# Optimization experiments

Hardware: AMD Instinct MI355X
Metric: run time of the kernel (lower is better)

## Reference

```python
import jax, jax.numpy as jnp
import numpy as np

B, NB, BS, F = 4, 16, 256, 1024   # batch, num_blocks, block_size, features
H, D = 16, 64                     # heads, head_dim
ROPE = 32                         # rope_rotary_dims


def rotate_every_two(x):
    x1 = x[..., ::2]
    x2 = x[..., 1::2]
    return jnp.stack([-x2, x1], axis=-1).reshape(x.shape)


def apply_rope(x, num_blocks, block_size):
    # x: [B, NB, BS, H, rope_dim]
    rope_dim = x.shape[-1]
    inv_freq = 1.0 / 10000.0 ** (jnp.arange(0, rope_dim, 2, dtype=jnp.float32) / rope_dim)
    pos = jnp.arange(num_blocks * block_size, dtype=jnp.float32)
    ang = pos[:, None] * inv_freq[None, :]                       # [S, rope_dim/2]
    sin = jnp.sin(ang).reshape(num_blocks, block_size, rope_dim // 2)
    cos = jnp.cos(ang).reshape(num_blocks, block_size, rope_dim // 2)
    sin = jnp.repeat(sin[None, :, :, None, :], 2, axis=-1)       # [1, NB, BS, 1, rope_dim]
    cos = jnp.repeat(cos[None, :, :, None, :], 2, axis=-1)
    return x * cos + rotate_every_two(x) * sin


def setup_inputs() -> dict:
    key = jax.random.key(0)
    ks = jax.random.split(key, 8)
    s_in = 1.0 / np.sqrt(F)
    s_out = 1.0 / np.sqrt(H * D)
    return {
        "inputs_q": jax.random.normal(ks[0], (B, NB, BS, F), jnp.float32),
        "inputs_kv": jax.random.normal(ks[1], (B, NB, BS, F), jnp.float32),
        "Wq": jax.random.normal(ks[2], (F, H, D), jnp.float32) * s_in,
        "bq": jnp.zeros((H, D), jnp.float32),
        "Wk": jax.random.normal(ks[3], (F, H, D), jnp.float32) * s_in,
        "bk": jnp.zeros((H, D), jnp.float32),
        "Wv": jax.random.normal(ks[4], (F, H, D), jnp.float32) * s_in,
        "bv": jnp.zeros((H, D), jnp.float32),
        "Wo": jax.random.normal(ks[5], (H, D, F), jnp.float32) * s_out,
        "bo": jnp.zeros((F,), jnp.float32),
    }


def reference(inputs_q, inputs_kv, Wq, bq, Wk, bk, Wv, bv, Wo, bo):
    # QKV projections: [B, NB, BS, F] x [F, H, D] -> [B, NB, BS, H, D]
    q = jnp.einsum("bnsf,fhd->bnshd", inputs_q, Wq) + bq
    k = jnp.einsum("bnsf,fhd->bnshd", inputs_kv, Wk) + bk
    v = jnp.einsum("bnsf,fhd->bnshd", inputs_kv, Wv) + bv

    # RoPE on first ROPE dims of head_dim (intended semantics per docstring)
    q_rot, q_pass = q[..., :ROPE], q[..., ROPE:]
    k_rot, k_pass = k[..., :ROPE], k[..., ROPE:]
    q = jnp.concatenate([apply_rope(q_rot, NB, BS), q_pass], axis=-1)
    k = jnp.concatenate([apply_rope(k_rot, NB, BS), k_pass], axis=-1)

    # block-local dot-product attention (flax nn.dot_product_attention semantics)
    q = q / jnp.sqrt(jnp.asarray(D, q.dtype))
    scores = jnp.einsum("bnqhd,bnkhd->bnhqk", q, k)              # [B, NB, H, BS, BS]
    weights = jax.nn.softmax(scores, axis=-1)
    x = jnp.einsum("bnhqk,bnkhd->bnqhd", weights, v)             # [B, NB, BS, H, D]

    # output projection over (heads, head_dim)
    out = jnp.einsum("bnqhd,hdf->bnqf", x, Wo) + bo              # [B, NB, BS, F]
    return out
```

## Files before the change

### kernel.cpp

```cpp
#include <hip/hip_runtime.h>

typedef __attribute__((ext_vector_type(4))) float f32x4;
typedef __attribute__((ext_vector_type(8))) short s16x8;
typedef __attribute__((ext_vector_type(4))) unsigned short u16x4;

struct F2 { float c, s; };

__device__ __forceinline__ unsigned short f2b(float f) {
  unsigned u = __builtin_bit_cast(unsigned, f);
  u += 0x7FFFu + ((u >> 16) & 1u);
  return (unsigned short)(u >> 16);
}
__device__ __forceinline__ void gll16(const void* g, void* l) {
  __builtin_amdgcn_global_load_lds(
      (const __attribute__((address_space(1))) unsigned int*)g,
      (__attribute__((address_space(3))) unsigned int*)l, 16, 0, 0);
}
__device__ __forceinline__ f32x4 mfma16(s16x8 a, s16x8 b, f32x4 c) {
  return __builtin_amdgcn_mfma_f32_16x16x32_bf16(a, b, c, 0, 0, 0);
}

__global__ void k_prep(const float* __restrict__ Xq, const float* __restrict__ Xkv,
                       unsigned short* __restrict__ Xqb, unsigned short* __restrict__ Xkvb,
                       F2* __restrict__ tab) {
  int b = blockIdx.x;
  if (b < 4096) {
    const float* src = (b < 2048) ? Xq : Xkv;
    unsigned short* dst = (b < 2048) ? Xqb : Xkvb;
    int i = (b & 2047) * 256 + threadIdx.x;
    for (; i < 4194304; i += 2048 * 256) {
      f32x4 v = ((const f32x4*)src)[i];
      u16x4 o;
      o.x = f2b(v.x); o.y = f2b(v.y); o.z = f2b(v.z); o.w = f2b(v.w);
      ((u16x4*)dst)[i] = o;
    }
  } else {
    int idx = (b - 4096) * 256 + threadIdx.x;
    int pos = idx >> 4, fi = idx & 15;
    double inv = exp((double)fi * (-9.210340371976184 / 16.0));
    double a = (double)pos * inv;
    F2 r; r.c = (float)cos(a); r.s = (float)sin(a);
    tab[idx] = r;
  }
}

__global__ void k_transpose(const float* __restrict__ wq,
                            const float* __restrict__ wk,
                            const float* __restrict__ wv,
                            const float* __restrict__ wo,
                            unsigned short* __restrict__ wtqkv,
                            unsigned short* __restrict__ wto) {
  __shared__ unsigned short tile[32][33];
  int z = blockIdx.z;
  const float* src = (z == 0) ? wq : (z == 1) ? wk : (z == 2) ? wv : wo;
  unsigned short* dst = (z < 3) ? (wtqkv + (size_t)z * 1048576) : wto;
  int bx = blockIdx.x * 32, by = blockIdx.y * 32;
  tile[threadIdx.y][threadIdx.x] = f2b(src[(size_t)(by + threadIdx.y) * 1024 + bx + threadIdx.x]);
  __syncthreads();
  dst[(size_t)(bx + threadIdx.y) * 1024 + by + threadIdx.x] = tile[threadIdx.x][threadIdx.y];
}

__device__ __forceinline__ void gemm_core(
    const unsigned short* __restrict__ Ag, const unsigned short* __restrict__ Bg,
    int m0, int n0, unsigned short* Sh, f32x4 (&acc)[8][4]) {
  const int tid = threadIdx.x, wid = tid >> 6, lane = tid & 63;
  const int fr = lane & 15, fg = lane >> 4, f7 = fr & 7;
  const int wm = wid >> 2, wn = wid & 3;
  const int rowoff = lane >> 3;
  const int lanecol = ((lane & 7) ^ rowoff) * 8;
  const int g0 = (fg ^ f7) * 8, g1 = ((4 + fg) ^ f7) * 8;

  auto SA = [&](int T, int ah) {
    unsigned short* dstb = Sh + (T & 1) * 32768;
#pragma unroll
    for (int i = 0; i < 2; ++i) {
      int rloc = ah * 128 + (wid * 2 + i) * 8;
      gll16(Ag + (size_t)(m0 + rloc + rowoff) * 1024 + T * 64 + lanecol, dstb + rloc * 64);
    }
  };
  auto SB = [&](int T, int bh) {
    unsigned short* dstb = Sh + (T & 1) * 32768 + 16384;
#pragma unroll
    for (int i = 0; i < 2; ++i) {
      int rloc = bh * 128 + (wid * 2 + i) * 8;
      gll16(Bg + (size_t)(n0 + rloc + rowoff) * 1024 + T * 64 + lanecol, dstb + rloc * 64);
    }
  };

  SA(0, 0); SA(0, 1); SB(0, 0); SB(0, 1); SA(1, 0); SA(1, 1);
  asm volatile("s_waitcnt vmcnt(4)" ::: "memory");
  __builtin_amdgcn_sched_barrier(0);
  __builtin_amdgcn_s_barrier();

  for (int t = 0; t < 16; ++t) {
    const unsigned short* bufA = Sh + (t & 1) * 32768;
    const unsigned short* bufB = bufA + 16384;
    s16x8 a0[4][2], a1[4][2], b0[2][2], b1[2][2];
#pragma unroll
    for (int mf = 0; mf < 4; ++mf) {
      const unsigned short* r = &bufA[(wm * 128 + mf * 16 + fr) * 64];
      a0[mf][0] = *(const s16x8*)&r[g0];
      a0[mf][1] = *(const s16x8*)&r[g1];
    }
#pragma unroll
    for (int nf = 0; nf < 2; ++nf) {
      const unsigned short* r = &bufB[(wn * 64 + nf * 16 + fr) * 64];
      b0[nf][0] = *(const s16x8*)&r[g0];
      b0[nf][1] = *(const s16x8*)&r[g1];
    }
    if (t + 1 < 16) SB(t + 1, 0);
    __builtin_amdgcn_s_barrier();
    asm volatile("s_waitcnt lgkmcnt(0)" ::: "memory");
    __builtin_amdgcn_sched_barrier(0);
    __builtin_amdgcn_s_setprio(1);
#pragma unroll
    for (int mf = 0; mf < 4; ++mf)
#pragma unroll
      for (int nf = 0; nf < 2; ++nf) {
        acc[mf][nf] = mfma16(a0[mf][0], b0[nf][0], acc[mf][nf]);
        acc[mf][nf] = mfma16(a0[mf][1], b0[nf][1], acc[mf][nf]);
      }
    __builtin_amdgcn_s_setprio(0);
    __builtin_amdgcn_s_barrier();
#pragma unroll
    for (int mf = 0; mf < 4; ++mf) {
      const unsigned short* r = &bufA[(wm * 128 + 64 + mf * 16 + fr) * 64];
      a1[mf][0] = *(const s16x8*)&r[g0];
      a1[mf][1] = *(const s16x8*)&r[g1];
    }
    if (t + 1 < 16) SB(t + 1, 1);
    __builtin_amdgcn_s_barrier();
    asm volatile("s_waitcnt lgkmcnt(0)" ::: "memory");
    __builtin_amdgcn_sched_barrier(0);
    __builtin_amdgcn_s_setprio(1);
#pragma unroll
    for (int mf = 0; mf < 4; ++mf)
#pragma unroll
      for (int nf = 0; nf < 2; ++nf) {
        acc[4 + mf][nf] = mfma16(a1[mf][0], b0[nf][0], acc[4 + mf][nf]);
        acc[4 + mf][nf] = mfma16(a1[mf][1], b0[nf][1], acc[4 + mf][nf]);
      }
    __builtin_amdgcn_s_setprio(0);
    __builtin_amdgcn_s_barrier();
#pragma unroll
    for (int nf = 0; nf < 2; ++nf) {
      const unsigned short* r = &bufB[(wn * 64 + 32 + nf * 16 + fr) * 64];
      b1[nf][0] = *(const s16x8*)&r[g0];
      b1[nf][1] = *(const s16x8*)&r[g1];
    }
    if (t + 2 < 16) SA(t + 2, 0);
    __builtin_amdgcn_s_barrier();
    asm volatile("s_waitcnt lgkmcnt(0)" ::: "memory");
    __builtin_amdgcn_sched_barrier(0);
    __builtin_amdgcn_s_setprio(1);
#pragma unroll
    for (int mf = 0; mf < 4; ++mf)
#pragma unroll
      for (int nf = 0; nf < 2; ++nf) {
        acc[4 + mf][2 + nf] = mfma16(a1[mf][0], b1[nf][0], acc[4 + mf][2 + nf]);
        acc[4 + mf][2 + nf] = mfma16(a1[mf][1], b1[nf][1], acc[4 + mf][2 + nf]);
      }
    __builtin_amdgcn_s_setprio(0);
    __builtin_amdgcn_s_barrier();
    if (t + 2 < 16) SA(t + 2, 1);
    if (t < 14) asm volatile("s_waitcnt vmcnt(4)" ::: "memory");
    else        asm volatile("s_waitcnt vmcnt(0)" ::: "memory");
    __builtin_amdgcn_sched_barrier(0);
    __builtin_amdgcn_s_barrier();
    __builtin_amdgcn_s_setprio(1);
#pragma unroll
    for (int mf = 0; mf < 4; ++mf)
#pragma unroll
      for (int nf = 0; nf < 2; ++nf) {
        acc[mf][2 + nf] = mfma16(a0[mf][0], b1[nf][0], acc[mf][2 + nf]);
        acc[mf][2 + nf] = mfma16(a0[mf][1], b1[nf][1], acc[mf][2 + nf]);
      }
    __builtin_amdgcn_s_setprio(0);
    __builtin_amdgcn_s_barrier();
  }
}

__global__ __launch_bounds__(512, 1) void k_qkv(
    const unsigned short* __restrict__ Xq,
    const unsigned short* __restrict__ Xkv,
    const unsigned short* __restrict__ WT,
    const float* __restrict__ bq,
    const float* __restrict__ bk,
    const float* __restrict__ bv,
    const F2* __restrict__ tab,
    unsigned short* __restrict__ qbuf,
    unsigned short* __restrict__ kbuf,
    unsigned short* __restrict__ vbuf) {
  __shared__ __align__(16) unsigned short S[65536];
  int bid = blockIdx.x;
  int swz = (bid & 7) * 96 + (bid >> 3);
  int mt = swz / 12, nt = swz % 12;
  int m0 = mt * 256, n0 = nt * 256;
  int which = n0 >> 10;
  const unsigned short* X = (which == 0) ? Xq : Xkv;
  const float* bias = (which == 0) ? bq : (which == 1) ? bk : bv;
  unsigned short* dst = (which == 0) ? qbuf : (which == 1) ? kbuf : vbuf;
  int n0l = n0 & 1023;
  int tid = threadIdx.x, wid = tid >> 6, lane = tid & 63;
  int fr = lane & 15, fg = lane >> 4;
  int wm = wid >> 2, wn = wid & 3;

  f32x4 acc[8][4] = {};
  gemm_core(X, WT, m0, n0, S, acc);

  unsigned short* W = S + wid * 8192;
  int hh = (n0l + wn * 64) >> 6;
  int bn = m0 >> 8;
#pragma unroll
  for (int nf = 0; nf < 4; ++nf) {
    int d = nf * 16 + fr;
    int col = n0l + wn * 64 + d;
    float bz = bias[col];
    bool rope = (which < 2) && (nf < 2);
#pragma unroll
    for (int mf = 0; mf < 8; ++mf) {
#pragma unroll
      for (int j = 0; j < 4; ++j) {
        int row = mf * 16 + fg * 4 + j;
        int mg = m0 + wm * 128 + row;
        float v = acc[mf][nf][j] + bz;
        if (rope) {
          float p = __shfl_xor(v, 1);
          F2 cs = tab[(mg & 4095) * 16 + (d >> 1)];
          v = (d & 1) ? fmaf(v, cs.c, p * cs.s) : fmaf(v, cs.c, -(p * cs.s));
        }
        if (which == 0) v *= 0.125f;
        W[row * 64 + (((d >> 3) ^ (row & 7)) << 3) + (d & 7)] = f2b(v);
      }
    }
  }
  asm volatile("s_waitcnt lgkmcnt(0)" ::: "memory");
  __builtin_amdgcn_sched_barrier(0);
  size_t gbase = ((size_t)(bn * 16 + hh) * 256 + wm * 128) * 64;
#pragma unroll
  for (int it = 0; it < 16; ++it) {
    int r = it * 8 + (lane >> 3);
    int ch = (lane & 7) ^ (r & 7);
    s16x8 vv = *(const s16x8*)&W[r * 64 + ch * 8];
    *(s16x8*)&dst[gbase + r * 64 + (lane & 7) * 8] = vv;
  }
}

__global__ __launch_bounds__(512, 1) void k_attn(
    const unsigned short* __restrict__ qbuf,
    const unsigned short* __restrict__ kbuf,
    const unsigned short* __restrict__ vbuf,
    unsigned short* __restrict__ xbuf) {
  __shared__ __align__(16) unsigned short Kl[256 * 64];
  __shared__ __align__(16) unsigned short Vt[64 * 264];
  __shared__ __align__(16) unsigned short Pl[8][16 * 264];
  int gb = blockIdx.x;
  size_t base = (size_t)gb * (256 * 64);
  const unsigned short* Q = qbuf + base;
  const unsigned short* K = kbuf + base;
  const unsigned short* V = vbuf + base;
  int bn = gb >> 4, h = gb & 15;
  int tid = threadIdx.x, wid = tid >> 6, lane = tid & 63;
  int fr = lane & 15, fg = lane >> 4;

#pragma unroll
  for (int tt = 0; tt < 4; ++tt) {
    int t = wid * 4 + tt;
    int r = t * 8 + (lane >> 3);
    int csrc = (lane & 7) ^ (r & 7);
    gll16(K + r * 64 + csrc * 8, &Kl[t * 512]);
  }
  {
    int rv = tid >> 1, chalf = (tid & 1) * 32;
#pragma unroll
    for (int c8 = 0; c8 < 4; ++c8) {
      s16x8 vv = *(const s16x8*)&V[rv * 64 + chalf + c8 * 8];
#pragma unroll
      for (int j = 0; j < 8; ++j)
        Vt[(chalf + c8 * 8 + j) * 264 + rv] = (unsigned short)vv[j];
    }
  }
  __syncthreads();

  unsigned short* P = Pl[wid];
  int f7 = fr & 7;
  int c0 = (fg ^ f7) * 8;
  int c1 = ((4 + fg) ^ f7) * 8;
  for (int mtile = 0; mtile < 2; ++mtile) {
    int q0 = wid * 32 + mtile * 16;
    s16x8 qa0 = *(const s16x8*)&Q[(q0 + fr) * 64 + fg * 8];
    s16x8 qa1 = *(const s16x8*)&Q[(q0 + fr) * 64 + 32 + fg * 8];
    f32x4 sc[16] = {};
#pragma unroll
    for (int nt = 0; nt < 16; ++nt) {
      int rr = nt * 16 + fr;
      s16x8 kb0 = *(const s16x8*)&Kl[rr * 64 + c0];
      sc[nt] = mfma16(qa0, kb0, sc[nt]);
      s16x8 kb1 = *(const s16x8*)&Kl[rr * 64 + c1];
      sc[nt] = mfma16(qa1, kb1, sc[nt]);
    }
    float rs[4];
#pragma unroll
    for (int j = 0; j < 4; ++j) {
      float m = sc[0][j];
#pragma unroll
      for (int nt = 1; nt < 16; ++nt) m = fmaxf(m, sc[nt][j]);
      m = fmaxf(m, __shfl_xor(m, 1));
      m = fmaxf(m, __shfl_xor(m, 2));
      m = fmaxf(m, __shfl_xor(m, 4));
      m = fmaxf(m, __shfl_xor(m, 8));
      float sum = 0.f;
#pragma unroll
      for (int nt = 0; nt < 16; ++nt) {
        float p = __expf(sc[nt][j] - m);
        sum += p;
        P[(fg * 4 + j) * 264 + nt * 16 + fr] = f2b(p);
      }
      sum += __shfl_xor(sum, 1);
      sum += __shfl_xor(sum, 2);
      sum += __shfl_xor(sum, 4);
      sum += __shfl_xor(sum, 8);
      rs[j] = 1.0f / sum;
    }
    f32x4 o[4] = {};
#pragma unroll
    for (int ks = 0; ks < 8; ++ks) {
      s16x8 pa = *(const s16x8*)&P[fr * 264 + ks * 32 + fg * 8];
#pragma unroll
      for (int nt = 0; nt < 4; ++nt) {
        s16x8 vb = *(const s16x8*)&Vt[(nt * 16 + fr) * 264 + ks * 32 + fg * 8];
        o[nt] = mfma16(pa, vb, o[nt]);
      }
    }
#pragma unroll
    for (int nt = 0; nt < 4; ++nt)
#pragma unroll
      for (int j = 0; j < 4; ++j) {
        int srow = q0 + fg * 4 + j;
        int d = nt * 16 + fr;
        xbuf[((size_t)(bn * 256 + srow)) * 1024 + h * 64 + d] = f2b(o[nt][j] * rs[j]);
      }
  }
}

__global__ __launch_bounds__(512, 1) void k_out(
    const unsigned short* __restrict__ Xb,
    const unsigned short* __restrict__ WT,
    const float* __restrict__ bo,
    float* __restrict__ out) {
  __shared__ __align__(16) unsigned short S[65536];
  int bid = blockIdx.x;
  int swz = (bid & 7) * 32 + (bid >> 3);
  int mt = swz >> 2, nt = swz & 3;
  int m0 = mt * 256, n0 = nt * 256;
  int tid = threadIdx.x, wid = tid >> 6, lane = tid & 63;
  int fr = lane & 15, fg = lane >> 4;
  int wm = wid >> 2, wn = wid & 3;

  f32x4 acc[8][4] = {};
  gemm_core(Xb, WT, m0, n0, S, acc);

  float* Wf = (float*)S + wid * 4096;
#pragma unroll
  for (int p = 0; p < 2; ++p) {
#pragma unroll
    for (int nf = 0; nf < 4; ++nf) {
      int d = nf * 16 + fr;
      float bz = bo[n0 + wn * 64 + d];
#pragma unroll
      for (int mf = 0; mf < 4; ++mf) {
#pragma unroll
        for (int j = 0; j < 4; ++j) {
          int row = mf * 16 + fg * 4 + j;
          Wf[row * 64 + d] = acc[p * 4 + mf][nf][j] + bz;
        }
      }
    }
    asm volatile("s_waitcnt lgkmcnt(0)" ::: "memory");
    __builtin_amdgcn_sched_barrier(0);
#pragma unroll
    for (int it = 0; it < 16; ++it) {
      int r = it * 4 + (lane >> 4);
      f32x4 vv = *(const f32x4*)&Wf[r * 64 + (lane & 15) * 4];
      int mg = m0 + wm * 128 + p * 64 + r;
      *(f32x4*)&out[(size_t)mg * 1024 + n0 + wn * 64 + (lane & 15) * 4] = vv;
    }
    asm volatile("s_waitcnt lgkmcnt(0)" ::: "memory");
    __builtin_amdgcn_sched_barrier(0);
  }
}

extern "C" void kernel_launch(void* const* d_in, const int* in_sizes, int n_in,
                              void* d_out, int out_size, void* d_ws, size_t ws_size,
                              hipStream_t stream) {
  const float* Xq  = (const float*)d_in[0];
  const float* Xkv = (const float*)d_in[1];
  const float* Wq  = (const float*)d_in[2];
  const float* bq  = (const float*)d_in[3];
  const float* Wk  = (const float*)d_in[4];
  const float* bk  = (const float*)d_in[5];
  const float* Wv  = (const float*)d_in[6];
  const float* bv  = (const float*)d_in[7];
  const float* Wo  = (const float*)d_in[8];
  const float* bo  = (const float*)d_in[9];
  float* out = (float*)d_out;

  char* ws = (char*)d_ws;
  size_t off = 0;
  F2* tab = (F2*)(ws + off);                           off += (size_t)65536 * sizeof(F2);
  unsigned short* WTqkv = (unsigned short*)(ws + off); off += (size_t)3 * 1048576 * 2;
  unsigned short* WTo   = (unsigned short*)(ws + off); off += (size_t)1048576 * 2;
  unsigned short* Xqb   = (unsigned short*)(ws + off); off += (size_t)16777216 * 2;
  unsigned short* Xkvb  = (unsigned short*)(ws + off); off += (size_t)16777216 * 2;
  unsigned short* qb = (unsigned short*)(ws + off); off += (size_t)16777216 * 2;
  unsigned short* kb = (unsigned short*)(ws + off); off += (size_t)16777216 * 2;
  unsigned short* vb = (unsigned short*)(ws + off); off += (size_t)16777216 * 2;
  unsigned short* xb = Xqb;

  k_prep<<<4352, 256, 0, stream>>>(Xq, Xkv, Xqb, Xkvb, tab);
  k_transpose<<<dim3(32, 32, 4), dim3(32, 32), 0, stream>>>(Wq, Wk, Wv, Wo, WTqkv, WTo);
  k_qkv<<<768, 512, 0, stream>>>(Xqb, Xkvb, WTqkv, bq, bk, bv, tab, qb, kb, vb);
  k_attn<<<1024, 512, 0, stream>>>(qb, kb, vb, xb);
  k_out<<<256, 512, 0, stream>>>(xb, WTo, bo, out);
}
```

Before: 279.2 us.

## Use 16 waves per GEMM block with smaller per-wave tiles

Result: no change. 282.5 us (+1.2%).

```diff
diff --git a/kernel.cpp b/kernel.cpp
--- a/kernel.cpp
+++ b/kernel.cpp
@@ -62,43 +62,39 @@
 
 __device__ __forceinline__ void gemm_core(
     const unsigned short* __restrict__ Ag, const unsigned short* __restrict__ Bg,
-    int m0, int n0, unsigned short* Sh, f32x4 (&acc)[8][4]) {
+    int m0, int n0, unsigned short* Sh, f32x4 (&acc)[4][4]) {
   const int tid = threadIdx.x, wid = tid >> 6, lane = tid & 63;
   const int fr = lane & 15, fg = lane >> 4, f7 = fr & 7;
   const int wm = wid >> 2, wn = wid & 3;
-  const int rowoff = lane >> 3;
-  const int lanecol = ((lane & 7) ^ rowoff) * 8;
   const int g0 = (fg ^ f7) * 8, g1 = ((4 + fg) ^ f7) * 8;
+  const int scp = lane & 7;
+  const int srow = wid * 8 + (lane >> 3);
 
   auto SA = [&](int T, int ah) {
     unsigned short* dstb = Sh + (T & 1) * 32768;
-#pragma unroll
-    for (int i = 0; i < 2; ++i) {
-      int rloc = ah * 128 + (wid * 2 + i) * 8;
-      gll16(Ag + (size_t)(m0 + rloc + rowoff) * 1024 + T * 64 + lanecol, dstb + rloc * 64);
-    }
+    int row = ah * 128 + srow;
+    gll16(Ag + (size_t)(m0 + row) * 1024 + T * 64 + (scp ^ (row & 7)) * 8,
+          dstb + (ah * 128 + wid * 8) * 64);
   };
   auto SB = [&](int T, int bh) {
     unsigned short* dstb = Sh + (T & 1) * 32768 + 16384;
-#pragma unroll
-    for (int i = 0; i < 2; ++i) {
-      int rloc = bh * 128 + (wid * 2 + i) * 8;
-      gll16(Bg + (size_t)(n0 + rloc + rowoff) * 1024 + T * 64 + lanecol, dstb + rloc * 64);
-    }
+    int row = bh * 128 + srow;
+    gll16(Bg + (size_t)(n0 + row) * 1024 + T * 64 + (scp ^ (row & 7)) * 8,
+          dstb + (bh * 128 + wid * 8) * 64);
   };
 
   SA(0, 0); SA(0, 1); SB(0, 0); SB(0, 1); SA(1, 0); SA(1, 1);
-  asm volatile("s_waitcnt vmcnt(4)" ::: "memory");
+  asm volatile("s_waitcnt vmcnt(2)" ::: "memory");
   __builtin_amdgcn_sched_barrier(0);
   __builtin_amdgcn_s_barrier();
 
   for (int t = 0; t < 16; ++t) {
     const unsigned short* bufA = Sh + (t & 1) * 32768;
     const unsigned short* bufB = bufA + 16384;
-    s16x8 a0[4][2], a1[4][2], b0[2][2], b1[2][2];
-#pragma unroll
-    for (int mf = 0; mf < 4; ++mf) {
-      const unsigned short* r = &bufA[(wm * 128 + mf * 16 + fr) * 64];
+    s16x8 a0[2][2], a1[2][2], b0[2][2], b1[2][2];
+#pragma unroll
+    for (int mf = 0; mf < 2; ++mf) {
+      const unsigned short* r = &bufA[(wm * 64 + mf * 16 + fr) * 64];
       a0[mf][0] = *(const s16x8*)&r[g0];
       a0[mf][1] = *(const s16x8*)&r[g1];
     }
@@ -114,7 +110,7 @@
     __builtin_amdgcn_sched_barrier(0);
     __builtin_amdgcn_s_setprio(1);
 #pragma unroll
-    for (int mf = 0; mf < 4; ++mf)
+    for (int mf = 0; mf < 2; ++mf)
 #pragma unroll
       for (int nf = 0; nf < 2; ++nf) {
         acc[mf][nf] = mfma16(a0[mf][0], b0[nf][0], acc[mf][nf]);
@@ -123,8 +119,8 @@
     __builtin_amdgcn_s_setprio(0);
     __builtin_amdgcn_s_barrier();
 #pragma unroll
-    for (int mf = 0; mf < 4; ++mf) {
-      const unsigned short* r = &bufA[(wm * 128 + 64 + mf * 16 + fr) * 64];
+    for (int mf = 0; mf < 2; ++mf) {
+      const unsigned short* r = &bufA[(wm * 64 + 32 + mf * 16 + fr) * 64];
       a1[mf][0] = *(const s16x8*)&r[g0];
       a1[mf][1] = *(const s16x8*)&r[g1];
     }
@@ -134,11 +130,11 @@
     __builtin_amdgcn_sched_barrier(0);
     __builtin_amdgcn_s_setprio(1);
 #pragma unroll
-    for (int mf = 0; mf < 4; ++mf)
+    for (int mf = 0; mf < 2; ++mf)
 #pragma unroll
       for (int nf = 0; nf < 2; ++nf) {
-        acc[4 + mf][nf] = mfma16(a1[mf][0], b0[nf][0], acc[4 + mf][nf]);
-        acc[4 + mf][nf] = mfma16(a1[mf][1], b0[nf][1], acc[4 + mf][nf]);
+        acc[2 + mf][nf] = mfma16(a1[mf][0], b0[nf][0], acc[2 + mf][nf]);
+        acc[2 + mf][nf] = mfma16(a1[mf][1], b0[nf][1], acc[2 + mf][nf]);
       }
     __builtin_amdgcn_s_setprio(0);
     __builtin_amdgcn_s_barrier();
@@ -154,22 +150,22 @@
     __builtin_amdgcn_sched_barrier(0);
     __builtin_amdgcn_s_setprio(1);
 #pragma unroll
-    for (int mf = 0; mf < 4; ++mf)
+    for (int mf = 0; mf < 2; ++mf)
 #pragma unroll
       for (int nf = 0; nf < 2; ++nf) {
-        acc[4 + mf][2 + nf] = mfma16(a1[mf][0], b1[nf][0], acc[4 + mf][2 + nf]);
-        acc[4 + mf][2 + nf] = mfma16(a1[mf][1], b1[nf][1], acc[4 + mf][2 + nf]);
+        acc[2 + mf][2 + nf] = mfma16(a1[mf][0], b1[nf][0], acc[2 + mf][2 + nf]);
+        acc[2 + mf][2 + nf] = mfma16(a1[mf][1], b1[nf][1], acc[2 + mf][2 + nf]);
       }
     __builtin_amdgcn_s_setprio(0);
     __builtin_amdgcn_s_barrier();
     if (t + 2 < 16) SA(t + 2, 1);
-    if (t < 14) asm volatile("s_waitcnt vmcnt(4)" ::: "memory");
+    if (t < 14) asm volatile("s_waitcnt vmcnt(2)" ::: "memory");
     else        asm volatile("s_waitcnt vmcnt(0)" ::: "memory");
     __builtin_amdgcn_sched_barrier(0);
     __builtin_amdgcn_s_barrier();
     __builtin_amdgcn_s_setprio(1);
 #pragma unroll
-    for (int mf = 0; mf < 4; ++mf)
+    for (int mf = 0; mf < 2; ++mf)
 #pragma unroll
       for (int nf = 0; nf < 2; ++nf) {
         acc[mf][2 + nf] = mfma16(a0[mf][0], b1[nf][0], acc[mf][2 + nf]);
@@ -180,7 +176,7 @@
   }
 }
 
-__global__ __launch_bounds__(512, 1) void k_qkv(
+__global__ __launch_bounds__(1024, 1) void k_qkv(
     const unsigned short* __restrict__ Xq,
     const unsigned short* __restrict__ Xkv,
     const unsigned short* __restrict__ WT,
@@ -205,10 +201,10 @@
   int fr = lane & 15, fg = lane >> 4;
   int wm = wid >> 2, wn = wid & 3;
 
-  f32x4 acc[8][4] = {};
+  f32x4 acc[4][4] = {};
   gemm_core(X, WT, m0, n0, S, acc);
 
-  unsigned short* W = S + wid * 8192;
+  unsigned short* W = S + wid * 4096;
   int hh = (n0l + wn * 64) >> 6;
   int bn = m0 >> 8;
 #pragma unroll
@@ -218,11 +214,11 @@
     float bz = bias[col];
     bool rope = (which < 2) && (nf < 2);
 #pragma unroll
-    for (int mf = 0; mf < 8; ++mf) {
+    for (int mf = 0; mf < 4; ++mf) {
 #pragma unroll
       for (int j = 0; j < 4; ++j) {
         int row = mf * 16 + fg * 4 + j;
-        int mg = m0 + wm * 128 + row;
+        int mg = m0 + wm * 64 + row;
         float v = acc[mf][nf][j] + bz;
         if (rope) {
           float p = __shfl_xor(v, 1);
@@ -236,9 +232,9 @@
   }
   asm volatile("s_waitcnt lgkmcnt(0)" ::: "memory");
   __builtin_amdgcn_sched_barrier(0);
-  size_t gbase = ((size_t)(bn * 16 + hh) * 256 + wm * 128) * 64;
-#pragma unroll
-  for (int it = 0; it < 16; ++it) {
+  size_t gbase = ((size_t)(bn * 16 + hh) * 256 + wm * 64) * 64;
+#pragma unroll
+  for (int it = 0; it < 8; ++it) {
     int r = it * 8 + (lane >> 3);
     int ch = (lane & 7) ^ (r & 7);
     s16x8 vv = *(const s16x8*)&W[r * 64 + ch * 8];
@@ -343,7 +339,7 @@
   }
 }
 
-__global__ __launch_bounds__(512, 1) void k_out(
+__global__ __launch_bounds__(1024, 1) void k_out(
     const unsigned short* __restrict__ Xb,
     const unsigned short* __restrict__ WT,
     const float* __restrict__ bo,
@@ -357,10 +353,10 @@
   int fr = lane & 15, fg = lane >> 4;
   int wm = wid >> 2, wn = wid & 3;
 
-  f32x4 acc[8][4] = {};
+  f32x4 acc[4][4] = {};
   gemm_core(Xb, WT, m0, n0, S, acc);
 
-  float* Wf = (float*)S + wid * 4096;
+  float* Wf = (float*)S + wid * 2048;
 #pragma unroll
   for (int p = 0; p < 2; ++p) {
 #pragma unroll
@@ -368,22 +364,25 @@
       int d = nf * 16 + fr;
       float bz = bo[n0 + wn * 64 + d];
 #pragma unroll
-      for (int mf = 0; mf < 4; ++mf) {
+      for (int mh = 0; mh < 2; ++mh) {
+        int mf = p * 2 + mh;
 #pragma unroll
         for (int j = 0; j < 4; ++j) {
-          int row = mf * 16 + fg * 4 + j;
-          Wf[row * 64 + d] = acc[p * 4 + mf][nf][j] + bz;
+          int rloc = mh * 16 + fg * 4 + j;
+          Wf[rloc * 64 + (((d >> 3) ^ (rloc & 7)) << 3) + (d & 7)] = acc[mf][nf][j] + bz;
         }
       }
     }
     asm volatile("s_waitcnt lgkmcnt(0)" ::: "memory");
     __builtin_amdgcn_sched_barrier(0);
 #pragma unroll
-    for (int it = 0; it < 16; ++it) {
-      int r = it * 4 + (lane >> 4);
-      f32x4 vv = *(const f32x4*)&Wf[r * 64 + (lane & 15) * 4];
-      int mg = m0 + wm * 128 + p * 64 + r;
-      *(f32x4*)&out[(size_t)mg * 1024 + n0 + wn * 64 + (lane & 15) * 4] = vv;
+    for (int it = 0; it < 8; ++it) {
+      int rloc = it * 4 + (lane >> 4);
+      int cpair = lane & 15;
+      int ch = (cpair >> 1) ^ (rloc & 7);
+      f32x4 vv = *(const f32x4*)&Wf[rloc * 64 + ch * 8 + (cpair & 1) * 4];
+      int mg = m0 + wm * 64 + p * 32 + rloc;
+      *(f32x4*)&out[(size_t)mg * 1024 + n0 + wn * 64 + cpair * 4] = vv;
     }
     asm volatile("s_waitcnt lgkmcnt(0)" ::: "memory");
     __builtin_amdgcn_sched_barrier(0);
@@ -419,7 +418,7 @@
 
   k_prep<<<4352, 256, 0, stream>>>(Xq, Xkv, Xqb, Xkvb, tab);
   k_transpose<<<dim3(32, 32, 4), dim3(32, 32), 0, stream>>>(Wq, Wk, Wv, Wo, WTqkv, WTo);
-  k_qkv<<<768, 512, 0, stream>>>(Xqb, Xkvb, WTqkv, bq, bk, bv, tab, qb, kb, vb);
+  k_qkv<<<768, 1024, 0, stream>>>(Xqb, Xkvb, WTqkv, bq, bk, bv, tab, qb, kb, vb);
   k_attn<<<1024, 512, 0, stream>>>(qb, kb, vb, xb);
-  k_out<<<256, 512, 0, stream>>>(xb, WTo, bo, out);
-}
+  k_out<<<256, 1024, 0, stream>>>(xb, WTo, bo, out);
+}
```

## Rewrite QKV GEMM with 128x128 tiles, 256 threads and simple single-buffer loop

Applied to the files above, without the earlier changes.

After: 261.0 us. -6.5%, faster.

```diff
diff --git a/kernel.cpp b/kernel.cpp
--- a/kernel.cpp
+++ b/kernel.cpp
@@ -60,127 +60,7 @@
   dst[(size_t)(bx + threadIdx.y) * 1024 + by + threadIdx.x] = tile[threadIdx.x][threadIdx.y];
 }
 
-__device__ __forceinline__ void gemm_core(
-    const unsigned short* __restrict__ Ag, const unsigned short* __restrict__ Bg,
-    int m0, int n0, unsigned short* Sh, f32x4 (&acc)[8][4]) {
-  const int tid = threadIdx.x, wid = tid >> 6, lane = tid & 63;
-  const int fr = lane & 15, fg = lane >> 4, f7 = fr & 7;
-  const int wm = wid >> 2, wn = wid & 3;
-  const int rowoff = lane >> 3;
-  const int lanecol = ((lane & 7) ^ rowoff) * 8;
-  const int g0 = (fg ^ f7) * 8, g1 = ((4 + fg) ^ f7) * 8;
-
-  auto SA = [&](int T, int ah) {
-    unsigned short* dstb = Sh + (T & 1) * 32768;
-#pragma unroll
-    for (int i = 0; i < 2; ++i) {
-      int rloc = ah * 128 + (wid * 2 + i) * 8;
-      gll16(Ag + (size_t)(m0 + rloc + rowoff) * 1024 + T * 64 + lanecol, dstb + rloc * 64);
-    }
-  };
-  auto SB = [&](int T, int bh) {
-    unsigned short* dstb = Sh + (T & 1) * 32768 + 16384;
-#pragma unroll
-    for (int i = 0; i < 2; ++i) {
-      int rloc = bh * 128 + (wid * 2 + i) * 8;
-      gll16(Bg + (size_t)(n0 + rloc + rowoff) * 1024 + T * 64 + lanecol, dstb + rloc * 64);
-    }
-  };
-
-  SA(0, 0); SA(0, 1); SB(0, 0); SB(0, 1); SA(1, 0); SA(1, 1);
-  asm volatile("s_waitcnt vmcnt(4)" ::: "memory");
-  __builtin_amdgcn_sched_barrier(0);
-  __builtin_amdgcn_s_barrier();
-
-  for (int t = 0; t < 16; ++t) {
-    const unsigned short* bufA = Sh + (t & 1) * 32768;
-    const unsigned short* bufB = bufA + 16384;
-    s16x8 a0[4][2], a1[4][2], b0[2][2], b1[2][2];
-#pragma unroll
-    for (int mf = 0; mf < 4; ++mf) {
-      const unsigned short* r = &bufA[(wm * 128 + mf * 16 + fr) * 64];
-      a0[mf][0] = *(const s16x8*)&r[g0];
-      a0[mf][1] = *(const s16x8*)&r[g1];
-    }
-#pragma unroll
-    for (int nf = 0; nf < 2; ++nf) {
-      const unsigned short* r = &bufB[(wn * 64 + nf * 16 + fr) * 64];
-      b0[nf][0] = *(const s16x8*)&r[g0];
-      b0[nf][1] = *(const s16x8*)&r[g1];
-    }
-    if (t + 1 < 16) SB(t + 1, 0);
-    __builtin_amdgcn_s_barrier();
-    asm volatile("s_waitcnt lgkmcnt(0)" ::: "memory");
-    __builtin_amdgcn_sched_barrier(0);
-    __builtin_amdgcn_s_setprio(1);
-#pragma unroll
-    for (int mf = 0; mf < 4; ++mf)
-#pragma unroll
-      for (int nf = 0; nf < 2; ++nf) {
-        acc[mf][nf] = mfma16(a0[mf][0], b0[nf][0], acc[mf][nf]);
-        acc[mf][nf] = mfma16(a0[mf][1], b0[nf][1], acc[mf][nf]);
-      }
-    __builtin_amdgcn_s_setprio(0);
-    __builtin_amdgcn_s_barrier();
-#pragma unroll
-    for (int mf = 0; mf < 4; ++mf) {
-      const unsigned short* r = &bufA[(wm * 128 + 64 + mf * 16 + fr) * 64];
-      a1[mf][0] = *(const s16x8*)&r[g0];
-      a1[mf][1] = *(const s16x8*)&r[g1];
-    }
-    if (t + 1 < 16) SB(t + 1, 1);
-    __builtin_amdgcn_s_barrier();
-    asm volatile("s_waitcnt lgkmcnt(0)" ::: "memory");
-    __builtin_amdgcn_sched_barrier(0);
-    __builtin_amdgcn_s_setprio(1);
-#pragma unroll
-    for (int mf = 0; mf < 4; ++mf)
-#pragma unroll
-      for (int nf = 0; nf < 2; ++nf) {
-        acc[4 + mf][nf] = mfma16(a1[mf][0], b0[nf][0], acc[4 + mf][nf]);
-        acc[4 + mf][nf] = mfma16(a1[mf][1], b0[nf][1], acc[4 + mf][nf]);
-      }
-    __builtin_amdgcn_s_setprio(0);
-    __builtin_amdgcn_s_barrier();
-#pragma unroll
-    for (int nf = 0; nf < 2; ++nf) {
-      const unsigned short* r = &bufB[(wn * 64 + 32 + nf * 16 + fr) * 64];
-      b1[nf][0] = *(const s16x8*)&r[g0];
-      b1[nf][1] = *(const s16x8*)&r[g1];
-    }
-    if (t + 2 < 16) SA(t + 2, 0);
-    __builtin_amdgcn_s_barrier();
-    asm volatile("s_waitcnt lgkmcnt(0)" ::: "memory");
-    __builtin_amdgcn_sched_barrier(0);
-    __builtin_amdgcn_s_setprio(1);
-#pragma unroll
-    for (int mf = 0; mf < 4; ++mf)
-#pragma unroll
-      for (int nf = 0; nf < 2; ++nf) {
-        acc[4 + mf][2 + nf] = mfma16(a1[mf][0], b1[nf][0], acc[4 + mf][2 + nf]);
-        acc[4 + mf][2 + nf] = mfma16(a1[mf][1], b1[nf][1], acc[4 + mf][2 + nf]);
-      }
-    __builtin_amdgcn_s_setprio(0);
-    __builtin_amdgcn_s_barrier();
-    if (t + 2 < 16) SA(t + 2, 1);
-    if (t < 14) asm volatile("s_waitcnt vmcnt(4)" ::: "memory");
-    else        asm volatile("s_waitcnt vmcnt(0)" ::: "memory");
-    __builtin_amdgcn_sched_barrier(0);
-    __builtin_amdgcn_s_barrier();
-    __builtin_amdgcn_s_setprio(1);
-#pragma unroll
-    for (int mf = 0; mf < 4; ++mf)
-#pragma unroll
-      for (int nf = 0; nf < 2; ++nf) {
-        acc[mf][2 + nf] = mfma16(a0[mf][0], b1[nf][0], acc[mf][2 + nf]);
-        acc[mf][2 + nf] = mfma16(a0[mf][1], b1[nf][1], acc[mf][2 + nf]);
-      }
-    __builtin_amdgcn_s_setprio(0);
-    __builtin_amdgcn_s_barrier();
-  }
-}
-
-__global__ __launch_bounds__(512, 1) void k_qkv(
+__global__ __launch_bounds__(256, 2) void k_qkv(
     const unsigned short* __restrict__ Xq,
     const unsigned short* __restrict__ Xkv,
     const unsigned short* __restrict__ WT,
@@ -191,38 +71,69 @@
     unsigned short* __restrict__ qbuf,
     unsigned short* __restrict__ kbuf,
     unsigned short* __restrict__ vbuf) {
-  __shared__ __align__(16) unsigned short S[65536];
+  __shared__ __align__(16) unsigned short S[16384];
+  unsigned short* Al = S;
+  unsigned short* Bl = S + 8192;
   int bid = blockIdx.x;
-  int swz = (bid & 7) * 96 + (bid >> 3);
-  int mt = swz / 12, nt = swz % 12;
-  int m0 = mt * 256, n0 = nt * 256;
+  int swz = (bid & 7) * 384 + (bid >> 3);
+  int mt = swz / 24, nt = swz % 24;
+  int m0 = mt * 128, n0 = nt * 128;
   int which = n0 >> 10;
   const unsigned short* X = (which == 0) ? Xq : Xkv;
   const float* bias = (which == 0) ? bq : (which == 1) ? bk : bv;
   unsigned short* dst = (which == 0) ? qbuf : (which == 1) ? kbuf : vbuf;
   int n0l = n0 & 1023;
   int tid = threadIdx.x, wid = tid >> 6, lane = tid & 63;
-  int fr = lane & 15, fg = lane >> 4;
-  int wm = wid >> 2, wn = wid & 3;
-
-  f32x4 acc[8][4] = {};
-  gemm_core(X, WT, m0, n0, S, acc);
-
-  unsigned short* W = S + wid * 8192;
-  int hh = (n0l + wn * 64) >> 6;
-  int bn = m0 >> 8;
+  int fr = lane & 15, fg = lane >> 4, f7 = fr & 7;
+  int wr = (wid >> 1) * 64, wc = (wid & 1) * 64;
+  int sr = lane >> 3, scp = lane & 7;
+  int g0 = (fg ^ f7) * 8, g1 = ((4 + fg) ^ f7) * 8;
+
+  f32x4 acc[4][4] = {};
+  for (int kt = 0; kt < 16; ++kt) {
+    int kb = kt * 64;
+#pragma unroll
+    for (int tt = 0; tt < 4; ++tt) {
+      int t = wid * 4 + tt;
+      int row = t * 8 + sr;
+      int cs = (scp ^ (row & 7)) * 8;
+      gll16(X  + (size_t)(m0 + row) * 1024 + kb + cs, &Al[t * 512]);
+      gll16(WT + (size_t)(n0 + row) * 1024 + kb + cs, &Bl[t * 512]);
+    }
+    __syncthreads();
+#pragma unroll
+    for (int ks = 0; ks < 2; ++ks) {
+      int gk = ks ? g1 : g0;
+      s16x8 af[4], bfr[4];
+#pragma unroll
+      for (int i = 0; i < 4; ++i) af[i]  = *(const s16x8*)&Al[(wr + i * 16 + fr) * 64 + gk];
+#pragma unroll
+      for (int i = 0; i < 4; ++i) bfr[i] = *(const s16x8*)&Bl[(wc + i * 16 + fr) * 64 + gk];
+#pragma unroll
+      for (int mi = 0; mi < 4; ++mi)
+#pragma unroll
+        for (int ni = 0; ni < 4; ++ni)
+          acc[mi][ni] = mfma16(af[mi], bfr[ni], acc[mi][ni]);
+    }
+    __syncthreads();
+  }
+
+  unsigned short* W = S + wid * 4096;
+  int hh = (n0l + wc) >> 6;
+  int rbase = m0 + wr;
+  int bn = rbase >> 8;
 #pragma unroll
   for (int nf = 0; nf < 4; ++nf) {
     int d = nf * 16 + fr;
-    int col = n0l + wn * 64 + d;
+    int col = n0l + wc + d;
     float bz = bias[col];
     bool rope = (which < 2) && (nf < 2);
 #pragma unroll
-    for (int mf = 0; mf < 8; ++mf) {
+    for (int mf = 0; mf < 4; ++mf) {
 #pragma unroll
       for (int j = 0; j < 4; ++j) {
         int row = mf * 16 + fg * 4 + j;
-        int mg = m0 + wm * 128 + row;
+        int mg = rbase + row;
         float v = acc[mf][nf][j] + bz;
         if (rope) {
           float p = __shfl_xor(v, 1);
@@ -236,13 +147,133 @@
   }
   asm volatile("s_waitcnt lgkmcnt(0)" ::: "memory");
   __builtin_amdgcn_sched_barrier(0);
-  size_t gbase = ((size_t)(bn * 16 + hh) * 256 + wm * 128) * 64;
-#pragma unroll
-  for (int it = 0; it < 16; ++it) {
+  size_t gbase = ((size_t)(bn * 16 + hh) * 256 + (rbase & 255)) * 64;
+#pragma unroll
+  for (int it = 0; it < 8; ++it) {
     int r = it * 8 + (lane >> 3);
     int ch = (lane & 7) ^ (r & 7);
     s16x8 vv = *(const s16x8*)&W[r * 64 + ch * 8];
     *(s16x8*)&dst[gbase + r * 64 + (lane & 7) * 8] = vv;
+  }
+}
+
+__device__ __forceinline__ void gemm_core(
+    const unsigned short* __restrict__ Ag, const unsigned short* __restrict__ Bg,
+    int m0, int n0, unsigned short* Sh, f32x4 (&acc)[8][4]) {
+  const int tid = threadIdx.x, wid = tid >> 6, lane = tid & 63;
+  const int fr = lane & 15, fg = lane >> 4, f7 = fr & 7;
+  const int wm = wid >> 2, wn = wid & 3;
+  const int rowoff = lane >> 3;
+  const int lanecol = ((lane & 7) ^ rowoff) * 8;
+  const int g0 = (fg ^ f7) * 8, g1 = ((4 + fg) ^ f7) * 8;
+
+  auto SA = [&](int T, int ah) {
+    unsigned short* dstb = Sh + (T & 1) * 32768;
+#pragma unroll
+    for (int i = 0; i < 2; ++i) {
+      int rloc = ah * 128 + (wid * 2 + i) * 8;
+      gll16(Ag + (size_t)(m0 + rloc + rowoff) * 1024 + T * 64 + lanecol, dstb + rloc * 64);
+    }
+  };
+  auto SB = [&](int T, int bh) {
+    unsigned short* dstb = Sh + (T & 1) * 32768 + 16384;
+#pragma unroll
+    for (int i = 0; i < 2; ++i) {
+      int rloc = bh * 128 + (wid * 2 + i) * 8;
+      gll16(Bg + (size_t)(n0 + rloc + rowoff) * 1024 + T * 64 + lanecol, dstb + rloc * 64);
+    }
+  };
+
+  SA(0, 0); SA(0, 1); SB(0, 0); SB(0, 1); SA(1, 0); SA(1, 1);
+  asm volatile("s_waitcnt vmcnt(4)" ::: "memory");
+  __builtin_amdgcn_sched_barrier(0);
+  __builtin_amdgcn_s_barrier();
+
+  for (int t = 0; t < 16; ++t) {
+    const unsigned short* bufA = Sh + (t & 1) * 32768;
+    const unsigned short* bufB = bufA + 16384;
+    s16x8 a0[4][2], a1[4][2], b0[2][2], b1[2][2];
+#pragma unroll
+    for (int mf = 0; mf < 4; ++mf) {
+      const unsigned short* r = &bufA[(wm * 128 + mf * 16 + fr) * 64];
+      a0[mf][0] = *(const s16x8*)&r[g0];
+      a0[mf][1] = *(const s16x8*)&r[g1];
+    }
+#pragma unroll
+    for (int nf = 0; nf < 2; ++nf) {
+      const unsigned short* r = &bufB[(wn * 64 + nf * 16 + fr) * 64];
+      b0[nf][0] = *(const s16x8*)&r[g0];
+      b0[nf][1] = *(const s16x8*)&r[g1];
+    }
+    if (t + 1 < 16) SB(t + 1, 0);
+    __builtin_amdgcn_s_barrier();
+    asm volatile("s_waitcnt lgkmcnt(0)" ::: "memory");
+    __builtin_amdgcn_sched_barrier(0);
+    __builtin_amdgcn_s_setprio(1);
+#pragma unroll
+    for (int mf = 0; mf < 4; ++mf)
+#pragma unroll
+      for (int nf = 0; nf < 2; ++nf) {
+        acc[mf][nf] = mfma16(a0[mf][0], b0[nf][0], acc[mf][nf]);
+        acc[mf][nf] = mfma16(a0[mf][1], b0[nf][1], acc[mf][nf]);
+      }
+    __builtin_amdgcn_s_setprio(0);
+    __builtin_amdgcn_s_barrier();
+#pragma unroll
+    for (int mf = 0; mf < 4; ++mf) {
+      const unsigned short* r = &bufA[(wm * 128 + 64 + mf * 16 + fr) * 64];
+      a1[mf][0] = *(const s16x8*)&r[g0];
+      a1[mf][1] = *(const s16x8*)&r[g1];
+    }
+    if (t + 1 < 16) SB(t + 1, 1);
+    __builtin_amdgcn_s_barrier();
+    asm volatile("s_waitcnt lgkmcnt(0)" ::: "memory");
+    __builtin_amdgcn_sched_barrier(0);
+    __builtin_amdgcn_s_setprio(1);
+#pragma unroll
+    for (int mf = 0; mf < 4; ++mf)
+#pragma unroll
+      for (int nf = 0; nf < 2; ++nf) {
+        acc[4 + mf][nf] = mfma16(a1[mf][0], b0[nf][0], acc[4 + mf][nf]);
+        acc[4 + mf][nf] = mfma16(a1[mf][1], b0[nf][1], acc[4 + mf][nf]);
+      }
+    __builtin_amdgcn_s_setprio(0);
+    __builtin_amdgcn_s_barrier();
+#pragma unroll
+    for (int nf = 0; nf < 2; ++nf) {
+      const unsigned short* r = &bufB[(wn * 64 + 32 + nf * 16 + fr) * 64];
+      b1[nf][0] = *(const s16x8*)&r[g0];
+      b1[nf][1] = *(const s16x8*)&r[g1];
+    }
+    if (t + 2 < 16) SA(t + 2, 0);
+    __builtin_amdgcn_s_barrier();
+    asm volatile("s_waitcnt lgkmcnt(0)" ::: "memory");
+    __builtin_amdgcn_sched_barrier(0);
+    __builtin_amdgcn_s_setprio(1);
+#pragma unroll
+    for (int mf = 0; mf < 4; ++mf)
+#pragma unroll
+      for (int nf = 0; nf < 2; ++nf) {
+        acc[4 + mf][2 + nf] = mfma16(a1[mf][0], b1[nf][0], acc[4 + mf][2 + nf]);
+        acc[4 + mf][2 + nf] = mfma16(a1[mf][1], b1[nf][1], acc[4 + mf][2 + nf]);
+      }
+    __builtin_amdgcn_s_setprio(0);
+    __builtin_amdgcn_s_barrier();
+    if (t + 2 < 16) SA(t + 2, 1);
+    if (t < 14) asm volatile("s_waitcnt vmcnt(4)" ::: "memory");
+    else        asm volatile("s_waitcnt vmcnt(0)" ::: "memory");
+    __builtin_amdgcn_sched_barrier(0);
+    __builtin_amdgcn_s_barrier();
+    __builtin_amdgcn_s_setprio(1);
+#pragma unroll
+    for (int mf = 0; mf < 4; ++mf)
+#pragma unroll
+      for (int nf = 0; nf < 2; ++nf) {
+        acc[mf][2 + nf] = mfma16(a0[mf][0], b1[nf][0], acc[mf][2 + nf]);
+        acc[mf][2 + nf] = mfma16(a0[mf][1], b1[nf][1], acc[mf][2 + nf]);
+      }
+    __builtin_amdgcn_s_setprio(0);
+    __builtin_amdgcn_s_barrier();
   }
 }
 
@@ -419,7 +450,7 @@
 
   k_prep<<<4352, 256, 0, stream>>>(Xq, Xkv, Xqb, Xkvb, tab);
   k_transpose<<<dim3(32, 32, 4), dim3(32, 32), 0, stream>>>(Wq, Wk, Wv, Wo, WTqkv, WTo);
-  k_qkv<<<768, 512, 0, stream>>>(Xqb, Xkvb, WTqkv, bq, bk, bv, tab, qb, kb, vb);
+  k_qkv<<<3072, 256, 0, stream>>>(Xqb, Xkvb, WTqkv, bq, bk, bv, tab, qb, kb, vb);
   k_attn<<<1024, 512, 0, stream>>>(qb, kb, vb, xb);
   k_out<<<256, 512, 0, stream>>>(xb, WTo, bo, out);
 }
```
